# Performance work log

Hardware: AMD Instinct MI355X
Metric: run time of the kernel (lower is better)

The kernel has to match this reference:

```python
import jax, jax.numpy as jnp
import numpy as np

N_NODES, N_EDGES, N_GRAPHS, H = 20000, 160000, 256, 128
EPS = 1e-5


def setup_inputs() -> dict:
    key = jax.random.key(0)
    it = iter(jax.random.split(key, 64))

    def nk():
        return next(it)

    def lin(fan_in, wshape, bshape):
        s = 1.0 / np.sqrt(fan_in)
        W = jax.random.uniform(nk(), wshape, jnp.float32, -s, s)
        b = jax.random.uniform(nk(), bshape, jnp.float32, -s, s)
        return W, b

    def bn_params(shape):
        g = 1.0 + 0.1 * jax.random.normal(nk(), shape, jnp.float32)
        b = 0.1 * jax.random.normal(nk(), shape, jnp.float32)
        m = 0.1 * jax.random.normal(nk(), shape, jnp.float32)
        v = jax.random.uniform(nk(), shape, jnp.float32, 0.5, 1.5)
        return g, b, m, v

    inp = {}
    inp["x"] = jax.random.normal(nk(), (N_NODES, 10), jnp.float32)
    inp["edge_attr"] = jax.random.normal(nk(), (N_EDGES, 3), jnp.float32)
    inp["edge_index"] = jax.random.randint(nk(), (2, N_EDGES), 0, N_NODES)
    inp["batch"] = jnp.sort(jax.random.randint(nk(), (N_NODES,), 0, N_GRAPHS))
    inp["W_node"], inp["b_node"] = lin(10, (10, H), (H,))
    inp["W_edge"], inp["b_edge"] = lin(3, (3, H), (H,))
    # 10 stacked CGConv layers: lin_f / lin_s each map [2H + H] -> H
    inp["Wf"], inp["bf"] = lin(3 * H, (10, 3 * H, H), (10, H))
    inp["Ws"], inp["bs"] = lin(3 * H, (10, 3 * H, H), (10, H))
    inp["bn_g"], inp["bn_b"], inp["bn_m"], inp["bn_v"] = bn_params((10, H))
    inp["W1"], inp["b1"] = lin(3 * H, (3 * H, 2 * H), (2 * H,))
    inp["bn1_g"], inp["bn1_b"], inp["bn1_m"], inp["bn1_v"] = bn_params((2 * H,))
    inp["W2"], inp["b2"] = lin(2 * H, (2 * H, H), (H,))
    inp["bn2_g"], inp["bn2_b"], inp["bn2_m"], inp["bn2_v"] = bn_params((H,))
    inp["W3"], inp["b3"] = lin(H, (H, H // 2), (H // 2,))
    inp["Wv"], inp["bv"] = lin(H // 2, (H // 2, 1), (1,))
    inp["W_en"], inp["b_en"] = lin(H // 2, (H // 2, 1), (1,))
    inp["Wd"], inp["bd"] = lin(H // 2, (H // 2, 1), (1,))
    inp["Wh"], inp["bh"] = lin(H // 2, (H // 2, 1), (1,))
    return inp


def reference(x, edge_attr, edge_index, batch, W_node, b_node, W_edge, b_edge,
              Wf, bf, Ws, bs, bn_g, bn_b, bn_m, bn_v,
              W1, b1, bn1_g, bn1_b, bn1_m, bn1_v,
              W2, b2, bn2_g, bn2_b, bn2_m, bn2_v,
              W3, b3, Wv, bv, W_en, b_en, Wd, bd, Wh, bh):
    h = jax.nn.relu(x @ W_node + b_node)             # [N, H]
    e = jax.nn.relu(edge_attr @ W_edge + b_edge)     # [E, H]
    src, dst = edge_index[0], edge_index[1]          # PyG: messages src -> dst
    n = h.shape[0]
    for i in range(10):  # fixed layer count, structurally distinct weights
        h_in = h
        z = jnp.concatenate([h[dst], h[src], e], axis=1)          # [E, 3H] = [x_i, x_j, e_ij]
        msg = jax.nn.sigmoid(z @ Wf[i] + bf[i]) * jax.nn.softplus(z @ Ws[i] + bs[i])
        h = h_in + jax.ops.segment_sum(msg, dst, num_segments=n)  # CGConv residual + add-aggr
        h = (h - bn_m[i]) * (bn_g[i] / jnp.sqrt(bn_v[i] + EPS)) + bn_b[i]  # BN (eval)
        h = jax.nn.relu(h)  # dropout is identity in eval
        if i % 2 == 1:
            h = h + h_in
    # global mean / max / add pooling over graphs
    s = jax.ops.segment_sum(h, batch, num_segments=N_GRAPHS)                     # [G, H]
    cnt = jax.ops.segment_sum(jnp.ones((n, 1), h.dtype), batch, num_segments=N_GRAPHS)
    mean = s / jnp.maximum(cnt, 1.0)
    mx = jax.ops.segment_max(h, batch, num_segments=N_GRAPHS)
    g = jnp.concatenate([mean, mx, s], axis=1)                                   # [G, 3H]
    g = jax.nn.relu((g @ W1 + b1 - bn1_m) * (bn1_g / jnp.sqrt(bn1_v + EPS)) + bn1_b)
    g = jax.nn.relu((g @ W2 + b2 - bn2_m) * (bn2_g / jnp.sqrt(bn2_v + EPS)) + bn2_b)
    g = jax.nn.relu(g @ W3 + b3)
    return (g @ Wv + bv, g @ W_en + b_en, g @ Wd + bd, g @ Wh + bh)
```

## Files before the change

### kernel.cpp

```cpp
#include <hip/hip_runtime.h>
#include <hip/hip_bf16.h>
#include <math.h>

#define NN 20000
#define NE 160000
#define NG 256
#define EPSV 1e-5f
#define NQB 2500

typedef short bf16x8 __attribute__((ext_vector_type(8)));
typedef unsigned short u16x8 __attribute__((ext_vector_type(8)));
typedef float f32x4 __attribute__((ext_vector_type(4)));

__device__ __forceinline__ unsigned short f2bf(float f){
  unsigned int u = __float_as_uint(f);
  unsigned int r = (u + 0x7fffu + ((u>>16)&1u)) >> 16;
  return (unsigned short)r;
}
__device__ __forceinline__ float bf2f(unsigned short h){
  return __uint_as_float(((unsigned int)h) << 16);
}
__device__ __forceinline__ float fastmsg(float f, float sv){
  float sg = __builtin_amdgcn_rcpf(1.0f + __expf(-f));
  float sp = fmaxf(sv, 0.0f) + __logf(1.0f + __expf(-fabsf(sv)));
  return sg * sp;
}

__global__ __launch_bounds__(256) void k_hist(const int* __restrict__ ei, int* __restrict__ deg){
  int e = blockIdx.x*256 + threadIdx.x;
  if (e < NE) atomicAdd(&deg[ei[NE+e]], 1);
}
__global__ __launch_bounds__(1024) void k_scan(const int* __restrict__ deg,
                                               int* __restrict__ start, int* __restrict__ cur){
  __shared__ int part[1024];
  int t = threadIdx.x;
  int base = t*20;
  int s = 0;
  for (int j=0;j<20;j++){ int i = base+j; if (i<NN) s += deg[i]; }
  part[t] = s; __syncthreads();
  for (int off=1; off<1024; off<<=1){
    int v = (t >= off) ? part[t-off] : 0;
    __syncthreads();
    part[t] += v;
    __syncthreads();
  }
  int run = (t>0) ? part[t-1] : 0;
  for (int j=0;j<20;j++){
    int i = base+j;
    if (i<NN){ start[i] = run; cur[i] = run; run += deg[i]; }
  }
}
__global__ __launch_bounds__(256) void k_scatter(
    const int* __restrict__ ei, const float* __restrict__ eattr,
    int* __restrict__ cur, int* __restrict__ ei_s, int* __restrict__ ei_d,
    float* __restrict__ ea_s){
  int e = blockIdx.x*256 + threadIdx.x;
  if (e >= NE) return;
  int d = ei[NE+e];
  int p = atomicAdd(&cur[d], 1);
  ei_s[p] = ei[e]; ei_d[p] = d;
  ea_s[p*3+0] = eattr[e*3+0];
  ea_s[p*3+1] = eattr[e*3+1];
  ea_s[p*3+2] = eattr[e*3+2];
}

__global__ __launch_bounds__(256) void k_pack_w(
    const float* __restrict__ Wf, const float* __restrict__ Ws,
    unsigned short* __restrict__ Wpk_hi, unsigned short* __restrict__ Wpk_md,
    unsigned short* __restrict__ Wpk_lo)
{
  int idx = blockIdx.x*256 + threadIdx.x;
  if (idx >= 122880) return;
  int l = idx & 63, ks = (idx>>6)&3, nt = (idx>>8)&7;
  int m = idx >> 11;
  int blk = m % 3, gL = m / 3;
  int g = gL & 1, L = gL >> 1;
  const float* src = (g ? Ws : Wf) + (size_t)L*384*128;
  size_t off = (size_t)m*16384 + (nt*4+ks)*512 + l*8;
  int col = nt*16 + (l&15), k0 = ks*32 + (l>>4)*8;
  #pragma unroll
  for (int j=0;j<8;j++){
    float w = src[(size_t)(blk*128 + k0 + j)*128 + col];
    unsigned short hi = f2bf(w);
    float r1 = w - bf2f(hi);
    unsigned short md = f2bf(r1);
    float r2 = r1 - bf2f(md);
    Wpk_hi[off+j] = hi;
    Wpk_md[off+j] = md;
    Wpk_lo[off+j] = f2bf(r2);
  }
}

__global__ __launch_bounds__(256) void k_embed_node(
    const float* __restrict__ x, const float* __restrict__ W, const float* __restrict__ b,
    float* __restrict__ h, float* __restrict__ hacc)
{
  int i = blockIdx.x*256 + threadIdx.x;
  if (i >= NN*128) return;
  int n = i >> 7, c = i & 127;
  float acc = b[c];
  const float* xr = x + n*10;
  #pragma unroll
  for (int k=0;k<10;k++) acc = fmaf(xr[k], W[k*128+c], acc);
  acc = fmaxf(acc, 0.0f);
  h[i] = acc; hacc[i] = acc;
}

__global__ __launch_bounds__(512,1) void k_nodeproj_mfma(
    const float* __restrict__ h,
    const unsigned short* __restrict__ Wpk_hi, const unsigned short* __restrict__ Wpk_md,
    const unsigned short* __restrict__ Wpk_lo,
    const float* __restrict__ bfv, const float* __restrict__ bsv,
    float* __restrict__ Pd, float* __restrict__ Ps)
{
  __shared__ unsigned short wsm[49152];
  int bid = blockIdx.x;
  int m_idx = bid / 157, nblk = bid - m_idx*157;
  int mm = (m_idx==0)?0:(m_idx==1)?1:(m_idx==2)?3:4;
  int t = threadIdx.x;
  {
    const unsigned short* s0 = Wpk_hi + (size_t)mm*16384;
    const unsigned short* s1 = Wpk_md + (size_t)mm*16384;
    const unsigned short* s2 = Wpk_lo + (size_t)mm*16384;
    #pragma unroll
    for (int ii=0; ii<4; ii++){
      int o = (t + ii*512)*8;
      *(u16x8*)(wsm + o)         = *(const u16x8*)(s0 + o);
      *(u16x8*)(wsm + 16384 + o) = *(const u16x8*)(s1 + o);
      *(u16x8*)(wsm + 32768 + o) = *(const u16x8*)(s2 + o);
    }
  }
  __syncthreads();
  int l = t & 63, w = t >> 6;
  int nb = nblk*128 + w*16;
  if (nb + 16 > NN) return;
  const float* hb = h + (size_t)(nb + (l&15))*128 + (l>>4)*8;
  bf16x8 ah[4], am[4], al[4];
  #pragma unroll
  for (int ks=0;ks<4;ks++){
    #pragma unroll
    for (int j=0;j<8;j++){
      float v = hb[ks*32 + j];
      unsigned short x0 = f2bf(v);
      float r1 = v - bf2f(x0);
      unsigned short x1 = f2bf(r1);
      float r2 = r1 - bf2f(x1);
      ah[ks][j] = (short)x0; am[ks][j] = (short)x1; al[ks][j] = (short)f2bf(r2);
    }
  }
  float* OUT = (m_idx & 1) ? Ps : Pd;
  int sel = (m_idx >= 2) ? 1 : 0;
  const float* bias = (m_idx==0) ? bfv : (m_idx==2) ? bsv : nullptr;
  int col0 = l & 15, rg = (l>>4)*4;
  #pragma unroll
  for (int nt=0; nt<8; nt++){
    f32x4 c = {0.f,0.f,0.f,0.f};
    #pragma unroll
    for (int ks=0;ks<4;ks++){
      int fo = (nt*4+ks)*512 + l*8;
      bf16x8 bh = *(const bf16x8*)(wsm + fo);
      bf16x8 bm = *(const bf16x8*)(wsm + 16384 + fo);
      bf16x8 bl = *(const bf16x8*)(wsm + 32768 + fo);
      c = __builtin_amdgcn_mfma_f32_16x16x32_bf16(al[ks], bh, c, 0,0,0);
      c = __builtin_amdgcn_mfma_f32_16x16x32_bf16(am[ks], bm, c, 0,0,0);
      c = __builtin_amdgcn_mfma_f32_16x16x32_bf16(ah[ks], bl, c, 0,0,0);
      c = __builtin_amdgcn_mfma_f32_16x16x32_bf16(am[ks], bh, c, 0,0,0);
      c = __builtin_amdgcn_mfma_f32_16x16x32_bf16(ah[ks], bm, c, 0,0,0);
      c = __builtin_amdgcn_mfma_f32_16x16x32_bf16(ah[ks], bh, c, 0,0,0);
    }
    float bb = bias ? bias[nt*16+col0] : 0.0f;
    #pragma unroll
    for (int r=0;r<4;r++)
      OUT[(size_t)(nb+rg+r)*256 + (nt*16+col0)*2 + sel] = c[r] + bb;
  }
}

__global__ __launch_bounds__(256,4) void k_edge_mfma(
    const float* __restrict__ ea_s, const float* __restrict__ W_edge,
    const float* __restrict__ b_edge,
    const unsigned short* __restrict__ Wpk_hi,
    const unsigned short* __restrict__ Wpk_md,
    const int* __restrict__ ei_s, const int* __restrict__ ei_d,
    const float* __restrict__ Pd, const float* __restrict__ Ps,
    float* __restrict__ hacc)
{
  __shared__ float wlds[512];
  __shared__ unsigned short bfr[16384];
  int bid = blockIdx.x;
  int q = bid / NQB, eg = bid - q*NQB;
  int t = threadIdx.x;
  for (int i=t;i<512;i+=256) wlds[i] = (i<384)? W_edge[i] : b_edge[i-384];
  #pragma unroll
  for (int ii=0; ii<8; ii++){
    int idx = t + ii*256;
    int f = idx >> 6;
    int off = (idx & 63) * 8;
    int g = f >> 4, term = (f>>3)&1, ntl = (f>>2)&1, ks = f&3;
    const unsigned short* src = (term ? Wpk_md : Wpk_hi)
        + (size_t)(g?5:2)*16384 + (size_t)((((q*2+ntl)*4+ks)*512) + off);
    *(u16x8*)(bfr + f*512 + off) = *(const u16x8*)src;
  }
  __syncthreads();
  int l = t & 63, w = t >> 6;
  int e0 = eg*64;
  int row_edge = e0 + w*16 + (l&15);
  float a0 = ea_s[row_edge*3+0], a1 = ea_s[row_edge*3+1], a2 = ea_s[row_edge*3+2];
  int cbase = (l>>4)*8;
  bf16x8 ah[4], al[4];
  #pragma unroll
  for (int ks=0;ks<4;ks++){
    #pragma unroll
    for (int j=0;j<8;j++){
      int c = cbase + ks*32 + j;
      float v = fmaf(a0, wlds[c], fmaf(a1, wlds[128+c], fmaf(a2, wlds[256+c], wlds[384+c])));
      v = fmaxf(v, 0.0f);
      unsigned short hi = f2bf(v);
      ah[ks][j] = (short)hi;
      al[ks][j] = (short)f2bf(v - bf2f(hi));
    }
  }
  f32x4 accf[2], accs[2];
  #pragma unroll
  for (int ntl=0; ntl<2; ntl++){
    f32x4 cf = {0.f,0.f,0.f,0.f}, cs = {0.f,0.f,0.f,0.f};
    #pragma unroll
    for (int ks=0; ks<4; ks++){
      bf16x8 bh = *(const bf16x8*)(bfr + ((0<<4)|(0<<3)|(ntl<<2)|ks)*512 + l*8);
      bf16x8 bm = *(const bf16x8*)(bfr + ((0<<4)|(1<<3)|(ntl<<2)|ks)*512 + l*8);
      cf = __builtin_amdgcn_mfma_f32_16x16x32_bf16(ah[ks], bh, cf, 0,0,0);
      cf = __builtin_amdgcn_mfma_f32_16x16x32_bf16(ah[ks], bm, cf, 0,0,0);
      cf = __builtin_amdgcn_mfma_f32_16x16x32_bf16(al[ks], bh, cf, 0,0,0);
      bf16x8 sh = *(const bf16x8*)(bfr + ((1<<4)|(0<<3)|(ntl<<2)|ks)*512 + l*8);
      bf16x8 sm = *(const bf16x8*)(bfr + ((1<<4)|(1<<3)|(ntl<<2)|ks)*512 + l*8);
      cs = __builtin_amdgcn_mfma_f32_16x16x32_bf16(ah[ks], sh, cs, 0,0,0);
      cs = __builtin_amdgcn_mfma_f32_16x16x32_bf16(ah[ks], sm, cs, 0,0,0);
      cs = __builtin_amdgcn_mfma_f32_16x16x32_bf16(al[ks], sh, cs, 0,0,0);
    }
    accf[ntl] = cf; accs[ntl] = cs;
  }
  int eb = e0 + w*16, col0 = l & 15, rg = (l>>4)*4;
  int cA = (q*2+0)*16 + col0;
  int cB = (q*2+1)*16 + col0;
  int prev_d = -1;
  float m0 = 0.f, m1 = 0.f;
  float2 pd0, pd1;
  #pragma unroll
  for (int r=0;r<4;r++){
    int p = eb + rg + r;
    int s = ei_s[p], d = ei_d[p];
    if (d != prev_d){
      if (prev_d >= 0){
        atomicAdd(hacc + (size_t)prev_d*128 + cA, m0);
        atomicAdd(hacc + (size_t)prev_d*128 + cB, m1);
      }
      prev_d = d;
      pd0 = *(const float2*)(Pd + (size_t)d*256 + cA*2);
      pd1 = *(const float2*)(Pd + (size_t)d*256 + cB*2);
      m0 = 0.f; m1 = 0.f;
    }
    float2 ps0 = *(const float2*)(Ps + (size_t)s*256 + cA*2);
    float2 ps1 = *(const float2*)(Ps + (size_t)s*256 + cB*2);
    m0 += fastmsg(accf[0][r] + pd0.x + ps0.x, accs[0][r] + pd0.y + ps0.y);
    m1 += fastmsg(accf[1][r] + pd1.x + ps1.x, accs[1][r] + pd1.y + ps1.y);
  }
  atomicAdd(hacc + (size_t)prev_d*128 + cA, m0);
  atomicAdd(hacc + (size_t)prev_d*128 + cB, m1);
}

__global__ __launch_bounds__(256) void k_bn(
    const float* __restrict__ hacc, const float* __restrict__ hin,
    const float* __restrict__ gam, const float* __restrict__ bet,
    const float* __restrict__ mu, const float* __restrict__ var,
    float* __restrict__ hout, float* __restrict__ haccout, int addres)
{
  int i = blockIdx.x*256 + threadIdx.x;
  if (i >= NN*128) return;
  int c = i & 127;
  float scale = gam[c]*rsqrtf(var[c]+EPSV);
  float tv = (hacc[i]-mu[c])*scale + bet[c];
  tv = fmaxf(tv, 0.0f);
  if (addres) tv += hin[i];
  hout[i] = tv; haccout[i] = tv;
}

__global__ __launch_bounds__(256) void k_pool(
    const float* __restrict__ h, const int* __restrict__ batch,
    float* __restrict__ psum, float* __restrict__ pmax, float* __restrict__ pcnt)
{
  int i = blockIdx.x*256 + threadIdx.x;
  if (i >= NN*128) return;
  int n = i >> 7, c = i & 127;
  int b = batch[n];
  float v = h[i];
  atomicAdd(&psum[b*128+c], v);
  atomicMax((unsigned int*)&pmax[b*128+c], __float_as_uint(v));
  if (c == 0) atomicAdd(&pcnt[b], 1.0f);
}

__global__ __launch_bounds__(256) void k_mlp1(
    const float* __restrict__ psum, const float* __restrict__ pmax, const float* __restrict__ pcnt,
    const float* __restrict__ W1, const float* __restrict__ b1,
    const float* __restrict__ g1g, const float* __restrict__ g1b,
    const float* __restrict__ g1m, const float* __restrict__ g1v,
    float* __restrict__ out)
{
  int i = blockIdx.x*256 + threadIdx.x;
  int g = i >> 8, c = i & 255;
  float inv = 1.0f / fmaxf(pcnt[g], 1.0f);
  float acc = b1[c];
  for (int k=0;k<128;k++) acc = fmaf(psum[g*128+k]*inv, W1[k*256+c], acc);
  for (int k=0;k<128;k++) acc = fmaf(pmax[g*128+k],     W1[(128+k)*256+c], acc);
  for (int k=0;k<128;k++) acc = fmaf(psum[g*128+k],     W1[(256+k)*256+c], acc);
  float scale = g1g[c]*rsqrtf(g1v[c]+EPSV);
  acc = (acc - g1m[c])*scale + g1b[c];
  out[i] = fmaxf(acc, 0.0f);
}

__global__ __launch_bounds__(256) void k_mlp2(
    const float* __restrict__ g1, const float* __restrict__ W2, const float* __restrict__ b2,
    const float* __restrict__ g2g, const float* __restrict__ g2b,
    const float* __restrict__ g2m, const float* __restrict__ g2v,
    float* __restrict__ out)
{
  int i = blockIdx.x*256 + threadIdx.x;
  int g = i >> 7, c = i & 127;
  float acc = b2[c];
  for (int k=0;k<256;k++) acc = fmaf(g1[g*256+k], W2[k*128+c], acc);
  float scale = g2g[c]*rsqrtf(g2v[c]+EPSV);
  acc = (acc - g2m[c])*scale + g2b[c];
  out[i] = fmaxf(acc, 0.0f);
}

__global__ __launch_bounds__(256) void k_mlp3(
    const float* __restrict__ g2, const float* __restrict__ W3, const float* __restrict__ b3,
    float* __restrict__ out)
{
  int i = blockIdx.x*256 + threadIdx.x;
  int g = i >> 6, c = i & 63;
  float acc = b3[c];
  for (int k=0;k<128;k++) acc = fmaf(g2[g*128+k], W3[k*64+c], acc);
  out[i] = fmaxf(acc, 0.0f);
}

__global__ __launch_bounds__(256) void k_heads(
    const float* __restrict__ g3,
    const float* __restrict__ Wv, const float* __restrict__ bv,
    const float* __restrict__ We, const float* __restrict__ be,
    const float* __restrict__ Wd, const float* __restrict__ bd,
    const float* __restrict__ Wh, const float* __restrict__ bh,
    float* __restrict__ out)
{
  int g = blockIdx.x*256 + threadIdx.x;
  if (g >= NG) return;
  float a0=bv[0], a1=be[0], a2=bd[0], a3=bh[0];
  for (int k=0;k<64;k++){
    float xv = g3[g*64+k];
    a0 = fmaf(xv, Wv[k], a0);
    a1 = fmaf(xv, We[k], a1);
    a2 = fmaf(xv, Wd[k], a2);
    a3 = fmaf(xv, Wh[k], a3);
  }
  out[g] = a0; out[NG+g] = a1; out[2*NG+g] = a2; out[3*NG+g] = a3;
}

extern "C" void kernel_launch(void* const* d_in, const int* in_sizes, int n_in,
                              void* d_out, int out_size, void* d_ws, size_t ws_size,
                              hipStream_t stream)
{
  const float* x         = (const float*)d_in[0];
  const float* edge_attr = (const float*)d_in[1];
  const int*   ei        = (const int*)d_in[2];
  const int*   batch     = (const int*)d_in[3];
  const float* W_node    = (const float*)d_in[4];
  const float* b_node    = (const float*)d_in[5];
  const float* W_edge    = (const float*)d_in[6];
  const float* b_edge    = (const float*)d_in[7];
  const float* Wf        = (const float*)d_in[8];
  const float* bf        = (const float*)d_in[9];
  const float* Ws        = (const float*)d_in[10];
  const float* bs        = (const float*)d_in[11];
  const float* bn_g      = (const float*)d_in[12];
  const float* bn_b      = (const float*)d_in[13];
  const float* bn_m      = (const float*)d_in[14];
  const float* bn_v      = (const float*)d_in[15];
  const float* W1        = (const float*)d_in[16];
  const float* b1        = (const float*)d_in[17];
  const float* bn1_g     = (const float*)d_in[18];
  const float* bn1_b     = (const float*)d_in[19];
  const float* bn1_m     = (const float*)d_in[20];
  const float* bn1_v     = (const float*)d_in[21];
  const float* W2        = (const float*)d_in[22];
  const float* b2        = (const float*)d_in[23];
  const float* bn2_g     = (const float*)d_in[24];
  const float* bn2_b     = (const float*)d_in[25];
  const float* bn2_m     = (const float*)d_in[26];
  const float* bn2_v     = (const float*)d_in[27];
  const float* W3        = (const float*)d_in[28];
  const float* b3        = (const float*)d_in[29];
  const float* Wv        = (const float*)d_in[30];
  const float* bv        = (const float*)d_in[31];
  const float* W_en      = (const float*)d_in[32];
  const float* b_en      = (const float*)d_in[33];
  const float* Wd        = (const float*)d_in[34];
  const float* bd        = (const float*)d_in[35];
  const float* Wh        = (const float*)d_in[36];
  const float* bh        = (const float*)d_in[37];

  float* wsf  = (float*)d_ws;
  float* h    = wsf;
  float* hacc = wsf + 2560000;
  float* Pd   = wsf + 5120000;
  float* Ps   = wsf + 10240000;
  unsigned short* Wpk_hi = (unsigned short*)(wsf + 15360000);
  unsigned short* Wpk_md = (unsigned short*)(wsf + 15851520);
  unsigned short* Wpk_lo = (unsigned short*)(wsf + 16343040);
  float* psum = wsf + 16834560;
  float* pmax = psum + 32768;
  float* pcnt = pmax + 32768;
  float* g1   = pcnt + 256;
  float* g2   = g1 + 65536;
  float* g3   = g2 + 32768;
  int*   deg  = (int*)(wsf + 16982272);
  int*   start= deg + 20000;
  int*   cur  = start + 20000;
  int*   ei_s = cur + 20000;
  int*   ei_d = ei_s + 160000;
  float* ea_s = (float*)(ei_d + 160000);

  hipMemsetAsync(deg, 0, 20000*sizeof(int), stream);
  k_hist<<<(NE+255)/256, 256, 0, stream>>>(ei, deg);
  k_scan<<<1, 1024, 0, stream>>>(deg, start, cur);
  k_scatter<<<(NE+255)/256, 256, 0, stream>>>(ei, edge_attr, cur, ei_s, ei_d, ea_s);

  k_pack_w<<<480, 256, 0, stream>>>(Wf, Ws, Wpk_hi, Wpk_md, Wpk_lo);
  k_embed_node<<<(NN*128+255)/256, 256, 0, stream>>>(x, W_node, b_node, h, hacc);
  hipMemsetAsync(psum, 0, (size_t)(32768+32768+256)*sizeof(float), stream);

  for (int i=0;i<10;i++){
    const unsigned short* WH = Wpk_hi + (size_t)i*6*16384;
    const unsigned short* WM = Wpk_md + (size_t)i*6*16384;
    const unsigned short* WL = Wpk_lo + (size_t)i*6*16384;
    k_nodeproj_mfma<<<628, 512, 0, stream>>>(h, WH, WM, WL,
        bf + i*128, bs + i*128, Pd, Ps);
    k_edge_mfma<<<4*NQB, 256, 0, stream>>>(ea_s, W_edge, b_edge,
        WH, WM, ei_s, ei_d, Pd, Ps, hacc);
    k_bn<<<(NN*128+255)/256, 256, 0, stream>>>(hacc, h,
        bn_g + i*128, bn_b + i*128, bn_m + i*128, bn_v + i*128, h, hacc, i&1);
  }

  k_pool<<<(NN*128+255)/256, 256, 0, stream>>>(h, batch, psum, pmax, pcnt);
  k_mlp1<<<(NG*256)/256, 256, 0, stream>>>(psum, pmax, pcnt, W1, b1, bn1_g, bn1_b, bn1_m, bn1_v, g1);
  k_mlp2<<<(NG*128)/256, 256, 0, stream>>>(g1, W2, b2, bn2_g, bn2_b, bn2_m, bn2_v, g2);
  k_mlp3<<<(NG*64)/256, 256, 0, stream>>>(g2, W3, b3, g3);
  k_heads<<<1, 256, 0, stream>>>(g3, Wv, bv, W_en, b_en, Wd, bd, Wh, bh, (float*)d_out);
}
```

Measured before the change: 1.424 ms.

## Precompute edge-embedding MFMA fragments once and pack src/dst indices

Adds a kernel that computes the ReLU edge embedding once and stores it as bf16 hi/lo MFMA fragments, which the per-layer edge kernel then loads instead of recomputing them in every layer. The path is used only when the workspace is large enough. Source and destination indices are packed into a single int2 array. The node projection kernel reads the low-order weight fragments straight from global memory, shrinking LDS use so two blocks can run per CU. The cost is extra global traffic for the fragment array, about 80 MB read in every layer.

```diff
diff --git a/kernel.cpp b/kernel.cpp
--- a/kernel.cpp
+++ b/kernel.cpp
@@ -52,16 +52,43 @@
 }
 __global__ __launch_bounds__(256) void k_scatter(
     const int* __restrict__ ei, const float* __restrict__ eattr,
-    int* __restrict__ cur, int* __restrict__ ei_s, int* __restrict__ ei_d,
-    float* __restrict__ ea_s){
+    int* __restrict__ cur, int2* __restrict__ esd, float* __restrict__ ea_s){
   int e = blockIdx.x*256 + threadIdx.x;
   if (e >= NE) return;
   int d = ei[NE+e];
   int p = atomicAdd(&cur[d], 1);
-  ei_s[p] = ei[e]; ei_d[p] = d;
+  esd[p] = make_int2(ei[e], d);
   ea_s[p*3+0] = eattr[e*3+0];
   ea_s[p*3+1] = eattr[e*3+1];
   ea_s[p*3+2] = eattr[e*3+2];
+}
+
+__global__ __launch_bounds__(256) void k_edge_frag(
+    const float* __restrict__ ea_s, const float* __restrict__ W_edge,
+    const float* __restrict__ b_edge, unsigned short* __restrict__ E_frag)
+{
+  int idx = blockIdx.x*256 + threadIdx.x;
+  if (idx >= 640000) return;
+  int g = idx >> 6, l = idx & 63;
+  int row = g*16 + (l&15);
+  float a0 = ea_s[row*3+0], a1 = ea_s[row*3+1], a2 = ea_s[row*3+2];
+  int cbase = (l>>4)*8;
+  unsigned short* dst = E_frag + (size_t)g*4096 + l*8;
+  #pragma unroll
+  for (int ks=0;ks<4;ks++){
+    u16x8 hv, lv;
+    #pragma unroll
+    for (int j=0;j<8;j++){
+      int c = cbase + ks*32 + j;
+      float v = fmaf(a0, W_edge[c], fmaf(a1, W_edge[128+c], fmaf(a2, W_edge[256+c], b_edge[c])));
+      v = fmaxf(v, 0.0f);
+      unsigned short hi = f2bf(v);
+      hv[j] = hi;
+      lv[j] = f2bf(v - bf2f(hi));
+    }
+    *(u16x8*)(dst + ks*512) = hv;
+    *(u16x8*)(dst + 2048 + ks*512) = lv;
+  }
 }
 
 __global__ __launch_bounds__(256) void k_pack_w(
@@ -106,14 +133,14 @@
   h[i] = acc; hacc[i] = acc;
 }
 
-__global__ __launch_bounds__(512,1) void k_nodeproj_mfma(
+__global__ __launch_bounds__(512,2) void k_nodeproj_mfma(
     const float* __restrict__ h,
     const unsigned short* __restrict__ Wpk_hi, const unsigned short* __restrict__ Wpk_md,
     const unsigned short* __restrict__ Wpk_lo,
     const float* __restrict__ bfv, const float* __restrict__ bsv,
     float* __restrict__ Pd, float* __restrict__ Ps)
 {
-  __shared__ unsigned short wsm[49152];
+  __shared__ unsigned short wsm[32768];
   int bid = blockIdx.x;
   int m_idx = bid / 157, nblk = bid - m_idx*157;
   int mm = (m_idx==0)?0:(m_idx==1)?1:(m_idx==2)?3:4;
@@ -121,13 +148,11 @@
   {
     const unsigned short* s0 = Wpk_hi + (size_t)mm*16384;
     const unsigned short* s1 = Wpk_md + (size_t)mm*16384;
-    const unsigned short* s2 = Wpk_lo + (size_t)mm*16384;
     #pragma unroll
     for (int ii=0; ii<4; ii++){
       int o = (t + ii*512)*8;
       *(u16x8*)(wsm + o)         = *(const u16x8*)(s0 + o);
       *(u16x8*)(wsm + 16384 + o) = *(const u16x8*)(s1 + o);
-      *(u16x8*)(wsm + 32768 + o) = *(const u16x8*)(s2 + o);
     }
   }
   __syncthreads();
@@ -148,6 +173,7 @@
       ah[ks][j] = (short)x0; am[ks][j] = (short)x1; al[ks][j] = (short)f2bf(r2);
     }
   }
+  const unsigned short* wl = Wpk_lo + (size_t)mm*16384 + l*8;
   float* OUT = (m_idx & 1) ? Ps : Pd;
   int sel = (m_idx >= 2) ? 1 : 0;
   const float* bias = (m_idx==0) ? bfv : (m_idx==2) ? bsv : nullptr;
@@ -160,7 +186,7 @@
       int fo = (nt*4+ks)*512 + l*8;
       bf16x8 bh = *(const bf16x8*)(wsm + fo);
       bf16x8 bm = *(const bf16x8*)(wsm + 16384 + fo);
-      bf16x8 bl = *(const bf16x8*)(wsm + 32768 + fo);
+      bf16x8 bl = *(const bf16x8*)(wl + (nt*4+ks)*512);
       c = __builtin_amdgcn_mfma_f32_16x16x32_bf16(al[ks], bh, c, 0,0,0);
       c = __builtin_amdgcn_mfma_f32_16x16x32_bf16(am[ks], bm, c, 0,0,0);
       c = __builtin_amdgcn_mfma_f32_16x16x32_bf16(ah[ks], bl, c, 0,0,0);
@@ -175,12 +201,14 @@
   }
 }
 
+template<bool PRE>
 __global__ __launch_bounds__(256,4) void k_edge_mfma(
     const float* __restrict__ ea_s, const float* __restrict__ W_edge,
     const float* __restrict__ b_edge,
+    const unsigned short* __restrict__ E_frag,
     const unsigned short* __restrict__ Wpk_hi,
     const unsigned short* __restrict__ Wpk_md,
-    const int* __restrict__ ei_s, const int* __restrict__ ei_d,
+    const int2* __restrict__ esd,
     const float* __restrict__ Pd, const float* __restrict__ Ps,
     float* __restrict__ hacc)
 {
@@ -189,7 +217,8 @@
   int bid = blockIdx.x;
   int q = bid / NQB, eg = bid - q*NQB;
   int t = threadIdx.x;
-  for (int i=t;i<512;i+=256) wlds[i] = (i<384)? W_edge[i] : b_edge[i-384];
+  if (!PRE)
+    for (int i=t;i<512;i+=256) wlds[i] = (i<384)? W_edge[i] : b_edge[i-384];
   #pragma unroll
   for (int ii=0; ii<8; ii++){
     int idx = t + ii*256;
@@ -203,20 +232,29 @@
   __syncthreads();
   int l = t & 63, w = t >> 6;
   int e0 = eg*64;
-  int row_edge = e0 + w*16 + (l&15);
-  float a0 = ea_s[row_edge*3+0], a1 = ea_s[row_edge*3+1], a2 = ea_s[row_edge*3+2];
-  int cbase = (l>>4)*8;
   bf16x8 ah[4], al[4];
-  #pragma unroll
-  for (int ks=0;ks<4;ks++){
-    #pragma unroll
-    for (int j=0;j<8;j++){
-      int c = cbase + ks*32 + j;
-      float v = fmaf(a0, wlds[c], fmaf(a1, wlds[128+c], fmaf(a2, wlds[256+c], wlds[384+c])));
-      v = fmaxf(v, 0.0f);
-      unsigned short hi = f2bf(v);
-      ah[ks][j] = (short)hi;
-      al[ks][j] = (short)f2bf(v - bf2f(hi));
+  if (PRE) {
+    const unsigned short* ef = E_frag + (size_t)(eg*4 + w)*4096 + l*8;
+    #pragma unroll
+    for (int ks=0;ks<4;ks++){
+      ah[ks] = *(const bf16x8*)(ef + ks*512);
+      al[ks] = *(const bf16x8*)(ef + 2048 + ks*512);
+    }
+  } else {
+    int row_edge = e0 + w*16 + (l&15);
+    float a0 = ea_s[row_edge*3+0], a1 = ea_s[row_edge*3+1], a2 = ea_s[row_edge*3+2];
+    int cbase = (l>>4)*8;
+    #pragma unroll
+    for (int ks=0;ks<4;ks++){
+      #pragma unroll
+      for (int j=0;j<8;j++){
+        int c = cbase + ks*32 + j;
+        float v = fmaf(a0, wlds[c], fmaf(a1, wlds[128+c], fmaf(a2, wlds[256+c], wlds[384+c])));
+        v = fmaxf(v, 0.0f);
+        unsigned short hi = f2bf(v);
+        ah[ks][j] = (short)hi;
+        al[ks][j] = (short)f2bf(v - bf2f(hi));
+      }
     }
   }
   f32x4 accf[2], accs[2];
@@ -247,7 +285,8 @@
   #pragma unroll
   for (int r=0;r<4;r++){
     int p = eb + rg + r;
-    int s = ei_s[p], d = ei_d[p];
+    int2 sd = esd[p];
+    int s = sd.x, d = sd.y;
     if (d != prev_d){
       if (prev_d >= 0){
         atomicAdd(hacc + (size_t)prev_d*128 + cA, m0);
@@ -423,14 +462,17 @@
   int*   deg  = (int*)(wsf + 16982272);
   int*   start= deg + 20000;
   int*   cur  = start + 20000;
-  int*   ei_s = cur + 20000;
-  int*   ei_d = ei_s + 160000;
-  float* ea_s = (float*)(ei_d + 160000);
+  int2*  esd  = (int2*)(cur + 20000);
+  float* ea_s = (float*)(cur + 20000 + 320000);
+  unsigned short* E_frag = (unsigned short*)(wsf + 17842272);
+  const size_t need_pre = (size_t)17842272*4 + (size_t)40960000*2;
+  const bool PRE = ws_size >= need_pre;
 
   hipMemsetAsync(deg, 0, 20000*sizeof(int), stream);
   k_hist<<<(NE+255)/256, 256, 0, stream>>>(ei, deg);
   k_scan<<<1, 1024, 0, stream>>>(deg, start, cur);
-  k_scatter<<<(NE+255)/256, 256, 0, stream>>>(ei, edge_attr, cur, ei_s, ei_d, ea_s);
+  k_scatter<<<(NE+255)/256, 256, 0, stream>>>(ei, edge_attr, cur, esd, ea_s);
+  if (PRE) k_edge_frag<<<2500, 256, 0, stream>>>(ea_s, W_edge, b_edge, E_frag);
 
   k_pack_w<<<480, 256, 0, stream>>>(Wf, Ws, Wpk_hi, Wpk_md, Wpk_lo);
   k_embed_node<<<(NN*128+255)/256, 256, 0, stream>>>(x, W_node, b_node, h, hacc);
@@ -442,8 +484,12 @@
     const unsigned short* WL = Wpk_lo + (size_t)i*6*16384;
     k_nodeproj_mfma<<<628, 512, 0, stream>>>(h, WH, WM, WL,
         bf + i*128, bs + i*128, Pd, Ps);
-    k_edge_mfma<<<4*NQB, 256, 0, stream>>>(ea_s, W_edge, b_edge,
-        WH, WM, ei_s, ei_d, Pd, Ps, hacc);
+    if (PRE)
+      k_edge_mfma<true><<<4*NQB, 256, 0, stream>>>(ea_s, W_edge, b_edge, E_frag,
+          WH, WM, esd, Pd, Ps, hacc);
+    else
+      k_edge_mfma<false><<<4*NQB, 256, 0, stream>>>(ea_s, W_edge, b_edge, E_frag,
+          WH, WM, esd, Pd, Ps, hacc);
     k_bn<<<(NN*128+255)/256, 256, 0, stream>>>(hacc, h,
         bn_g + i*128, bn_b + i*128, bn_m + i*128, bn_v + i*128, h, hacc, i&1);
   }
```

New measurement: 1.439 ms. No clear change (+1.0%).
